# Kernel tuning notes

Hardware: AMD Instinct MI355X
Metric: run time of the kernel (lower is better)

The kernel has to match this reference:

```python
import jax, jax.numpy as jnp
import numpy as np


def setup_inputs() -> dict:
    key = jax.random.key(0)
    M, N = 2048, 16384
    x = jax.random.normal(key, (M, N), dtype=jnp.float32)
    # expk per DREAMPlace get_expk: exp(-j*pi*n/(2N)) stored as [N, 2] = (cos, -sin)
    ang = jnp.arange(N, dtype=jnp.float32) * np.float32(np.pi / (2.0 * N))
    expk = jnp.stack([jnp.cos(ang), -jnp.sin(ang)], axis=-1)
    return {"x": x, "expk": expk}


def reference(x, expk):
    """IDXCT: y_k = Re{ sum_{n=0}^{N-1} x_n * exp(j*pi/(2N) * n * (2k+1)) }.

    O(N log N) via the FFT trick:
      y_k = Re{ sum_n [x_n * exp(j*pi*n/(2N))] * exp(j*2*pi*n*k/(2N)) }
          = 2N * Re{ IFFT_{2N}(zero-padded v)[k] },  v_n = x_n * conj(expk_n)
    """
    N = x.shape[-1]
    # expk encodes exp(-j*pi*n/(2N)); we need its conjugate exp(+j*pi*n/(2N))
    v = x * (expk[..., 0] - 1j * expk[..., 1])  # complex64, [M, N]
    V = jnp.fft.ifft(v, n=2 * N, axis=-1)       # zero-padded to 2N
    y = (2 * N) * jnp.real(V[..., :N])
    return y.astype(x.dtype)
```

## Files before the change

### kernel.cpp

```cpp
#include <hip/hip_runtime.h>

#define PI_F 3.14159265358979323846f

constexpr int N_COLS = 16384;
constexpr int HALF   = 8192;
constexpr int NT     = 1024;

__host__ __device__ constexpr int Sc(int p) {
    return p ^ ((p >> 4) & 15) ^ ((p >> 8) & 31);
}
__host__ __device__ constexpr int br3(int c) {
    return ((c & 1) << 2) | (c & 2) | ((c & 4) >> 2);
}

__global__ __launch_bounds__(NT, 8)
void idxct_kernel(const float* __restrict__ x,
                  const float* __restrict__ expk,
                  float* __restrict__ y)
{
    __shared__ float2 zs[HALF];

    const int row = blockIdx.x;
    const float* __restrict__ xr = x + (size_t)row * N_COLS;
    float* __restrict__ yr       = y + (size_t)row * N_COLS;
    const int t = threadIdx.x;
    const float x0 = xr[0];
    const float2* __restrict__ ek2 = (const float2*)expk;

    const int spt = Sc((int)(__brev((unsigned)t) >> 22) << 3);
    #pragma unroll
    for (int i = 0; i < HALF / NT; ++i) {
        int k = t + i * NT;
        float vkr, vki, c0, s0;
        {
            float2 e = ek2[k];
            c0 = e.x; s0 = -e.y;
            if (k == 0) { vkr = x0; vki = 0.0f; }
            else {
                float a = xr[k], b = xr[N_COLS - k];
                vkr = a * c0 + b * s0;
                vki = a * s0 - b * c0;
            }
        }
        float wkr, wki;
        {
            int K = k + HALF;
            float2 e = ek2[K];
            float c = e.x, s = -e.y;
            float a = xr[K], b = xr[N_COLS - K];
            wkr = a * c + b * s;
            wki = a * s - b * c;
        }
        float dr = vkr - wkr, di = vki - wki;
        float cA = c0 * c0 - s0 * s0, sA = 2.0f * c0 * s0;
        float ec = cA * cA - sA * sA, es = 2.0f * cA * sA;
        float zr = (vkr + wkr) - (ec * di + es * dr);
        float zi = (vki + wki) + (ec * dr - es * di);
        zs[spt ^ br3(i)] = make_float2(zr, zi);
    }

    float2 T[5], T6;
    {
        float sn, cs;
        __sincosf((float)(t & 3)   * (PI_F / 8.0f),    &sn, &cs); T[0] = make_float2(cs, sn);
        __sincosf((float)(t & 15)  * (PI_F / 32.0f),   &sn, &cs); T[1] = make_float2(cs, sn);
        __sincosf((float)(t & 63)  * (PI_F / 128.0f),  &sn, &cs); T[2] = make_float2(cs, sn);
        __sincosf((float)(t & 255) * (PI_F / 512.0f),  &sn, &cs); T[3] = make_float2(cs, sn);
        __sincosf((float)t         * (PI_F / 2048.0f), &sn, &cs); T[4] = make_float2(cs, sn);
        __sincosf((float)t         * (PI_F / 4096.0f), &sn, &cs); T6   = make_float2(cs, sn);
    }

    __syncthreads();
    #pragma unroll
    for (int u = 0; u < 2; ++u) {
        int q = t + u * NT;
        int a0 = Sc(q << 2);
        int a1 = a0 ^ 1, a2i = a0 ^ 2, a3 = a0 ^ 3;
        float2 e0 = zs[a0], e1 = zs[a1], e2 = zs[a2i], e3 = zs[a3];
        float tr, ti;
        tr = e1.x;  ti = e1.y;  e1.x = e0.x - tr; e1.y = e0.y - ti; e0.x += tr; e0.y += ti;
        tr = e3.x;  ti = e3.y;  e3.x = e2.x - tr; e3.y = e2.y - ti; e2.x += tr; e2.y += ti;
        tr = e2.x;  ti = e2.y;  e2.x = e0.x - tr; e2.y = e0.y - ti; e0.x += tr; e0.y += ti;
        tr = -e3.y; ti = e3.x;  e3.x = e1.x - tr; e3.y = e1.y - ti; e1.x += tr; e1.y += ti;
        zs[a0]  = e0; zs[a1] = e1; zs[a2i] = e2; zs[a3] = e3;
    }

    #pragma unroll
    for (int p = 1; p < 6; ++p) {
        const int s = 1 << (2 * p);
        __syncthreads();
        const float c2 = T[p - 1].x, s2 = T[p - 1].y;
        const float c1 = c2 * c2 - s2 * s2;
        const float s1 = 2.0f * c2 * s2;
        #pragma unroll
        for (int u = 0; u < 2; ++u) {
            int q = t + u * NT;
            int j = q & (s - 1);
            int base = ((q >> (2 * p)) << (2 * p + 2)) + j;
            int a0  = Sc(base);
            int a1  = a0 ^ Sc(s);
            int a2i = a0 ^ Sc(2 * s);
            int a3  = a0 ^ Sc(3 * s);
            float2 e0 = zs[a0], e1 = zs[a1], e2 = zs[a2i], e3 = zs[a3];
            float tr, ti;
            tr = c1 * e1.x - s1 * e1.y; ti = c1 * e1.y + s1 * e1.x;
            e1.x = e0.x - tr; e1.y = e0.y - ti; e0.x += tr; e0.y += ti;
            tr = c1 * e3.x - s1 * e3.y; ti = c1 * e3.y + s1 * e3.x;
            e3.x = e2.x - tr; e3.y = e2.y - ti; e2.x += tr; e2.y += ti;
            tr = c2 * e2.x - s2 * e2.y; ti = c2 * e2.y + s2 * e2.x;
            e2.x = e0.x - tr; e2.y = e0.y - ti; e0.x += tr; e0.y += ti;
            tr = -s2 * e3.x - c2 * e3.y; ti = c2 * e3.x - s2 * e3.y;
            e3.x = e1.x - tr; e3.y = e1.y - ti; e1.x += tr; e1.y += ti;
            zs[a0]  = e0; zs[a1] = e1; zs[a2i] = e2; zs[a3] = e3;
        }
    }
    __syncthreads();

    {
        const float2 C4 = make_float2(0.99999970586288222f,
                                      7.6699031874270453e-4f);
        constexpr float RT = 0.70710678118654752440f;
        const int sct = Sc(t);
        const int scr = sct ^ Sc(1023);
        #pragma unroll
        for (int i = 0; i < 4; ++i) {
            const int m   = t + NT * i;
            const int am  = sct ^ Sc(NT * i);
            const int ar  = scr ^ Sc(NT * (3 - i));
            const int am2 = am ^ Sc(4096);
            const int ar2 = ar ^ Sc(4096);
            float2 um = zs[am];
            float2 vm = zs[am2];
            float2 ur = zs[ar];
            float2 wr = zs[ar2];
            float exr, exi;
            if      (i == 0) { exr = T6.x;                 exi = T6.y; }
            else if (i == 1) { exr = (T6.x - T6.y) * RT;   exi = (T6.x + T6.y) * RT; }
            else if (i == 2) { exr = -T6.y;                exi = T6.x; }
            else             { exr = -(T6.x + T6.y) * RT;  exi = (T6.x - T6.y) * RT; }
            float Fr = exr * C4.x - exi * C4.y;
            float Fi = exr * C4.y + exi * C4.x;
            float cwr = -Fr, swr = Fi;
            float trm = exr * vm.x - exi * vm.y;
            float tim = exr * vm.y + exi * vm.x;
            float trr = cwr * wr.x - swr * wr.y;
            float tir = cwr * wr.y + swr * wr.x;
            float4 o;
            o.x = 0.5f * ((um.x + trm) + x0);
            o.y = 0.5f * ((ur.y - tir) + x0);
            o.z = 0.5f * ((um.y + tim) + x0);
            o.w = 0.5f * ((ur.x - trr) + x0);
            *reinterpret_cast<float4*>(yr + 4 * m) = o;
        }
    }
}

extern "C" void kernel_launch(void* const* d_in, const int* in_sizes, int n_in,
                              void* d_out, int out_size, void* d_ws, size_t ws_size,
                              hipStream_t stream)
{
    const float* x    = (const float*)d_in[0];
    const float* expk = (const float*)d_in[1];
    float* y          = (float*)d_out;
    const int M = in_sizes[0] / N_COLS;
    idxct_kernel<<<dim3(M), dim3(NT), 0, stream>>>(x, expk, y);
}
```

Before: 252.2 us.

## Fuse first radix-8 FFT stage into registers and drop final combine pass

Each thread now performs a radix-8 butterfly on the eight values it already wrote, directly in registers. The remaining stages become five radix-4 shared-memory passes, and the last pass carries an extra rotation for the second half. The final output step then just reads finished FFT values without a separate radix-2 twiddle stage. This aims to remove one shared-memory pass and barrier plus output-stage twiddle arithmetic, at the cost of a new register-heavy stage and revised twiddle indexing.

```diff
diff --git a/kernel.cpp b/kernel.cpp
--- a/kernel.cpp
+++ b/kernel.cpp
@@ -11,6 +11,52 @@
 }
 __host__ __device__ constexpr int br3(int c) {
     return ((c & 1) << 2) | (c & 2) | ((c & 4) >> 2);
+}
+
+__device__ __forceinline__ void bf2(float2& a, float2& b) {
+    float tr = b.x, ti = b.y;
+    b.x = a.x - tr; b.y = a.y - ti;
+    a.x += tr; a.y += ti;
+}
+__device__ __forceinline__ void bf4(float2& e0, float2& e1, float2& e2, float2& e3,
+                                    float cw, float sw) {
+    float c1 = cw * cw - sw * sw;
+    float s1 = 2.0f * cw * sw;
+    float tr, ti;
+    tr = c1 * e1.x - s1 * e1.y; ti = c1 * e1.y + s1 * e1.x;
+    e1.x = e0.x - tr; e1.y = e0.y - ti; e0.x += tr; e0.y += ti;
+    tr = c1 * e3.x - s1 * e3.y; ti = c1 * e3.y + s1 * e3.x;
+    e3.x = e2.x - tr; e3.y = e2.y - ti; e2.x += tr; e2.y += ti;
+    tr = cw * e2.x - sw * e2.y; ti = cw * e2.y + sw * e2.x;
+    e2.x = e0.x - tr; e2.y = e0.y - ti; e0.x += tr; e0.y += ti;
+    tr = -sw * e3.x - cw * e3.y; ti = cw * e3.x - sw * e3.y;
+    e3.x = e1.x - tr; e3.y = e1.y - ti; e1.x += tr; e1.y += ti;
+}
+
+template<int LS, bool ROT>
+__device__ __forceinline__ void pass4(float2* __restrict__ zs, int t,
+                                      float c2, float s2) {
+    const int s = 1 << LS;
+    #pragma unroll
+    for (int u = 0; u < 2; ++u) {
+        float cw = c2, sw = s2;
+        if (ROT && u == 1) {
+            constexpr float RT = 0.70710678118654752440f;
+            float cr = (cw - sw) * RT;
+            float sr = (cw + sw) * RT;
+            cw = cr; sw = sr;
+        }
+        int q = t + u * NT;
+        int j = q & (s - 1);
+        int base = ((q >> LS) << (LS + 2)) | j;
+        int a0  = Sc(base);
+        int a1  = a0 ^ Sc(s);
+        int a2i = a0 ^ Sc(2 * s);
+        int a3  = a0 ^ Sc(3 * s);
+        float2 e0 = zs[a0], e1 = zs[a1], e2 = zs[a2i], e3 = zs[a3];
+        bf4(e0, e1, e2, e3, cw, sw);
+        zs[a0] = e0; zs[a1] = e1; zs[a2i] = e2; zs[a3] = e3;
+    }
 }
 
 __global__ __launch_bounds__(NT, 8)
@@ -59,97 +105,54 @@
         zs[spt ^ br3(i)] = make_float2(zr, zi);
     }
 
-    float2 T[5], T6;
+    {
+        float2 v[8];
+        #pragma unroll
+        for (int o = 0; o < 8; ++o) v[o] = zs[spt ^ o];
+        bf2(v[0], v[1]); bf2(v[2], v[3]); bf2(v[4], v[5]); bf2(v[6], v[7]);
+        constexpr float RT = 0.70710678118654752440f;
+        bf4(v[0], v[2], v[4], v[6], 1.0f, 0.0f);
+        bf4(v[1], v[3], v[5], v[7], RT, RT);
+        #pragma unroll
+        for (int o = 0; o < 8; ++o) zs[spt ^ o] = v[o];
+    }
+
+    float2 T0, T1, T2, T3, T4;
     {
         float sn, cs;
-        __sincosf((float)(t & 3)   * (PI_F / 8.0f),    &sn, &cs); T[0] = make_float2(cs, sn);
-        __sincosf((float)(t & 15)  * (PI_F / 32.0f),   &sn, &cs); T[1] = make_float2(cs, sn);
-        __sincosf((float)(t & 63)  * (PI_F / 128.0f),  &sn, &cs); T[2] = make_float2(cs, sn);
-        __sincosf((float)(t & 255) * (PI_F / 512.0f),  &sn, &cs); T[3] = make_float2(cs, sn);
-        __sincosf((float)t         * (PI_F / 2048.0f), &sn, &cs); T[4] = make_float2(cs, sn);
-        __sincosf((float)t         * (PI_F / 4096.0f), &sn, &cs); T6   = make_float2(cs, sn);
+        __sincosf((float)(t & 7)   * (PI_F / 16.0f),   &sn, &cs); T0 = make_float2(cs, sn);
+        __sincosf((float)(t & 31)  * (PI_F / 64.0f),   &sn, &cs); T1 = make_float2(cs, sn);
+        __sincosf((float)(t & 127) * (PI_F / 256.0f),  &sn, &cs); T2 = make_float2(cs, sn);
+        __sincosf((float)(t & 511) * (PI_F / 1024.0f), &sn, &cs); T3 = make_float2(cs, sn);
+        __sincosf((float)t         * (PI_F / 4096.0f), &sn, &cs); T4 = make_float2(cs, sn);
     }
 
     __syncthreads();
-    #pragma unroll
-    for (int u = 0; u < 2; ++u) {
-        int q = t + u * NT;
-        int a0 = Sc(q << 2);
-        int a1 = a0 ^ 1, a2i = a0 ^ 2, a3 = a0 ^ 3;
-        float2 e0 = zs[a0], e1 = zs[a1], e2 = zs[a2i], e3 = zs[a3];
-        float tr, ti;
-        tr = e1.x;  ti = e1.y;  e1.x = e0.x - tr; e1.y = e0.y - ti; e0.x += tr; e0.y += ti;
-        tr = e3.x;  ti = e3.y;  e3.x = e2.x - tr; e3.y = e2.y - ti; e2.x += tr; e2.y += ti;
-        tr = e2.x;  ti = e2.y;  e2.x = e0.x - tr; e2.y = e0.y - ti; e0.x += tr; e0.y += ti;
-        tr = -e3.y; ti = e3.x;  e3.x = e1.x - tr; e3.y = e1.y - ti; e1.x += tr; e1.y += ti;
-        zs[a0]  = e0; zs[a1] = e1; zs[a2i] = e2; zs[a3] = e3;
-    }
-
-    #pragma unroll
-    for (int p = 1; p < 6; ++p) {
-        const int s = 1 << (2 * p);
-        __syncthreads();
-        const float c2 = T[p - 1].x, s2 = T[p - 1].y;
-        const float c1 = c2 * c2 - s2 * s2;
-        const float s1 = 2.0f * c2 * s2;
-        #pragma unroll
-        for (int u = 0; u < 2; ++u) {
-            int q = t + u * NT;
-            int j = q & (s - 1);
-            int base = ((q >> (2 * p)) << (2 * p + 2)) + j;
-            int a0  = Sc(base);
-            int a1  = a0 ^ Sc(s);
-            int a2i = a0 ^ Sc(2 * s);
-            int a3  = a0 ^ Sc(3 * s);
-            float2 e0 = zs[a0], e1 = zs[a1], e2 = zs[a2i], e3 = zs[a3];
-            float tr, ti;
-            tr = c1 * e1.x - s1 * e1.y; ti = c1 * e1.y + s1 * e1.x;
-            e1.x = e0.x - tr; e1.y = e0.y - ti; e0.x += tr; e0.y += ti;
-            tr = c1 * e3.x - s1 * e3.y; ti = c1 * e3.y + s1 * e3.x;
-            e3.x = e2.x - tr; e3.y = e2.y - ti; e2.x += tr; e2.y += ti;
-            tr = c2 * e2.x - s2 * e2.y; ti = c2 * e2.y + s2 * e2.x;
-            e2.x = e0.x - tr; e2.y = e0.y - ti; e0.x += tr; e0.y += ti;
-            tr = -s2 * e3.x - c2 * e3.y; ti = c2 * e3.x - s2 * e3.y;
-            e3.x = e1.x - tr; e3.y = e1.y - ti; e1.x += tr; e1.y += ti;
-            zs[a0]  = e0; zs[a1] = e1; zs[a2i] = e2; zs[a3] = e3;
-        }
-    }
+    pass4<3,  false>(zs, t, T0.x, T0.y);
+    __syncthreads();
+    pass4<5,  false>(zs, t, T1.x, T1.y);
+    __syncthreads();
+    pass4<7,  false>(zs, t, T2.x, T2.y);
+    __syncthreads();
+    pass4<9,  false>(zs, t, T3.x, T3.y);
+    __syncthreads();
+    pass4<11, true >(zs, t, T4.x, T4.y);
     __syncthreads();
 
     {
-        const float2 C4 = make_float2(0.99999970586288222f,
-                                      7.6699031874270453e-4f);
-        constexpr float RT = 0.70710678118654752440f;
         const int sct = Sc(t);
-        const int scr = sct ^ Sc(1023);
         #pragma unroll
         for (int i = 0; i < 4; ++i) {
-            const int m   = t + NT * i;
-            const int am  = sct ^ Sc(NT * i);
-            const int ar  = scr ^ Sc(NT * (3 - i));
-            const int am2 = am ^ Sc(4096);
-            const int ar2 = ar ^ Sc(4096);
-            float2 um = zs[am];
-            float2 vm = zs[am2];
-            float2 ur = zs[ar];
-            float2 wr = zs[ar2];
-            float exr, exi;
-            if      (i == 0) { exr = T6.x;                 exi = T6.y; }
-            else if (i == 1) { exr = (T6.x - T6.y) * RT;   exi = (T6.x + T6.y) * RT; }
-            else if (i == 2) { exr = -T6.y;                exi = T6.x; }
-            else             { exr = -(T6.x + T6.y) * RT;  exi = (T6.x - T6.y) * RT; }
-            float Fr = exr * C4.x - exi * C4.y;
-            float Fi = exr * C4.y + exi * C4.x;
-            float cwr = -Fr, swr = Fi;
-            float trm = exr * vm.x - exi * vm.y;
-            float tim = exr * vm.y + exi * vm.x;
-            float trr = cwr * wr.x - swr * wr.y;
-            float tir = cwr * wr.y + swr * wr.x;
+            const int m  = t + NT * i;
+            const int am = sct ^ Sc(NT * i);
+            const int ao = am ^ Sc(8191);
+            float2 zm = zs[am];
+            float2 zo = zs[ao];
             float4 o;
-            o.x = 0.5f * ((um.x + trm) + x0);
-            o.y = 0.5f * ((ur.y - tir) + x0);
-            o.z = 0.5f * ((um.y + tim) + x0);
-            o.w = 0.5f * ((ur.x - trr) + x0);
+            o.x = 0.5f * (zm.x + x0);
+            o.y = 0.5f * (zo.y + x0);
+            o.z = 0.5f * (zm.y + x0);
+            o.w = 0.5f * (zo.x + x0);
             *reinterpret_cast<float4*>(yr + 4 * m) = o;
         }
     }
```

After: 249.6 us. Within noise of the previous version (-1.0%).
